# Optimization experiments

Measured on AMD Instinct MI355X. Metric: run time of the kernel, lower is better.

The kernel has to match this reference:

```python
import jax, jax.numpy as jnp
import numpy as np

B, L, D, H = 8, 1024, 1024, 16
DH = D // H  # 64


def setup_inputs() -> dict:
    key = jax.random.key(0)
    ks = jax.random.split(key, 6)
    x = jax.random.normal(ks[0], (B, L, D), dtype=jnp.float32)
    mask = jax.random.randint(ks[1], (1, L, L), 0, 2).astype(jnp.float32)
    # params initialized ~ normal(std=0.1) as in the module's _initialize
    Wk = jax.random.normal(ks[2], (D, D), dtype=jnp.float32) * 0.1
    Wv = jax.random.normal(ks[3], (D, D), dtype=jnp.float32) * 0.1
    Wq = jax.random.normal(ks[4], (D, D), dtype=jnp.float32) * 0.1
    Wo = jax.random.normal(ks[5], (D, D), dtype=jnp.float32) * 0.1
    return {"x": x, "mask": mask, "Wk": Wk, "Wv": Wv, "Wq": Wq, "Wo": Wo}


def reference(x, mask, Wk, Wv, Wq, Wo):
    # torch Linear: y = x @ W.T
    k = jnp.einsum('bld,ed->ble', x, Wk).reshape(B, L, H, DH)
    v = jnp.einsum('bld,ed->ble', x, Wv).reshape(B, L, H, DH)
    q = jnp.einsum('bld,ed->ble', x, Wq).reshape(B, L, H, DH)
    # explicit score matrix [B, H, L, L]
    scores = jnp.einsum('blhe,bmhe->bhlm', q, k)
    m = mask[:, None]  # (1, 1, L, L) broadcasts over batch and heads
    scores = scores * m - 1e9 * (1.0 - m)
    scale = np.float32(1.0 / np.sqrt(DH))
    weights = jax.nn.softmax(scores * scale, axis=-1)
    out = jnp.einsum('bhlm,bmhe->blhe', weights, v).reshape(B, L, D)
    out = jnp.einsum('bld,ed->ble', out, Wo)  # output_linear (n_heads > 1)
    return out
```

## Files before the change

kernel.cpp:

```cpp
#include <hip/hip_runtime.h>

#define B_  8
#define L_  1024
#define D_  1024
#define H_  16
#define DH_ 64

typedef unsigned short u16;
typedef __attribute__((ext_vector_type(8))) short short8;
typedef __attribute__((ext_vector_type(8))) _Float16 half8;
typedef __attribute__((ext_vector_type(4))) float floatx4;
typedef __attribute__((ext_vector_type(16))) float floatx16;

static __device__ __forceinline__ u16 f2bf(float f) {
  union { float f; unsigned u; } cv; cv.f = f;
  unsigned u = cv.u;
  return (u16)((u + 0x7fffu + ((u >> 16) & 1u)) >> 16);
}
static __device__ __forceinline__ u16 f2h(float f) {
  union { _Float16 h; u16 u; } cv; cv.h = (_Float16)f; return cv.u;
}
static __device__ __forceinline__ unsigned pack_bf2(float a, float b) {
  union { float f; unsigned u; } ua, ub; ua.f = a; ub.f = b;
  return __builtin_amdgcn_perm(ub.u + 0x8000u, ua.u + 0x8000u, 0x07060302u);
}

__global__ void cast_all(const float* __restrict__ x,  const float* __restrict__ wq,
                         const float* __restrict__ wk, const float* __restrict__ wv,
                         const float* __restrict__ wo, const float* __restrict__ mask,
                         u16* __restrict__ xf,  u16* __restrict__ wqf,
                         u16* __restrict__ wkf, u16* __restrict__ wvf,
                         u16* __restrict__ wof, float* __restrict__ biasP) {
  int blk = blockIdx.x;
  if (blk >= 12288) {
    int i = (blk - 12288) * 256 + threadIdx.x;
    int e = i & 3, lane = (i >> 2) & 63, rr = (i >> 8) & 3, t = (i >> 10) & 1;
    int c = (i >> 11) & 15, w = (i >> 15) & 3, qt = i >> 17;
    int kk  = e + 8 * rr + 4 * (lane >> 5);
    int row = qt * 128 + w * 32 + (lane & 31);
    int key = c * 64 + t * 32 + kk;
    biasP[i] = (mask[(size_t)row * L_ + key] - 1.0f) * 1.25e8f - 24.0f;
    return;
  }
  const float* src; u16* dst; int off;
  if (blk < 8192)       { src = x;  dst = xf;  off = blk; }
  else if (blk < 9216)  { src = wq; dst = wqf; off = blk - 8192; }
  else if (blk < 10240) { src = wk; dst = wkf; off = blk - 9216; }
  else if (blk < 11264) { src = wv; dst = wvf; off = blk - 10240; }
  else                  { src = wo; dst = wof; off = blk - 11264; }
  int i = off * 1024 + threadIdx.x * 4;
  float4 f = *(const float4*)(src + i);
  ushort4 r;
  r.x = f2h(f.x); r.y = f2h(f.y); r.z = f2h(f.z); r.w = f2h(f.w);
  *(ushort4*)(dst + i) = r;
}

typedef __attribute__((address_space(3))) void  lds_void;
typedef const __attribute__((address_space(1))) void g_void;
static __device__ __forceinline__ void load_lds16(const void* g, void* l) {
  __builtin_amdgcn_global_load_lds((g_void*)g, (lds_void*)l, 16, 0, 0);
}

__global__ __launch_bounds__(256) void gemm_qkv(const u16* __restrict__ A,
                                                const u16* __restrict__ wq,
                                                const u16* __restrict__ wk,
                                                const u16* __restrict__ wv,
                                                u16* __restrict__ qf,
                                                u16* __restrict__ kf,
                                                u16* __restrict__ vb) {
  const int K = D_, N = D_;
  int nb = blockIdx.x;
  const u16* Bw; u16* Cp; float scale; int obf;
  if (nb < 8)       { Bw = wq; Cp = qf; scale = 0.125f; obf = 0; }
  else if (nb < 16) { Bw = wk; Cp = kf; scale = 1.0f;   obf = 0; }
  else              { Bw = wv; Cp = vb; scale = 1.0f;   obf = 1; }
  const int n0 = (nb & 7) * 128;

  __shared__ u16 lA[128 * 32];
  __shared__ u16 lB[128 * 32];
  const int tid  = threadIdx.x;
  const int w    = tid >> 6;
  const int lane = tid & 63;
  const int m    = lane & 15;
  const int kg   = lane >> 4;
  const int m0   = blockIdx.y * 128;
  const int wm   = (w >> 1) * 64;
  const int wn   = (w & 1) * 64;
  const int rowS = tid >> 2;
  const int part = tid & 3;

  floatx4 acc[4][4];
#pragma unroll
  for (int i = 0; i < 4; ++i)
#pragma unroll
    for (int j = 0; j < 4; ++j)
#pragma unroll
      for (int r = 0; r < 4; ++r) acc[i][j][r] = 0.0f;

  for (int k0 = 0; k0 < K; k0 += 32) {
    __syncthreads();
#pragma unroll
    for (int rnd = 0; rnd < 2; ++rnd) {
      const u16* ga = A  + (size_t)(m0 + rnd * 64 + rowS) * K + k0 + part * 8;
      const u16* gb = Bw + (size_t)(n0 + rnd * 64 + rowS) * K + k0 + part * 8;
      load_lds16(ga, lA + rnd * 2048 + w * 512);
      load_lds16(gb, lB + rnd * 2048 + w * 512);
    }
    __syncthreads();

    half8 af[4], bf[4];
#pragma unroll
    for (int i = 0; i < 4; ++i) af[i] = *(const half8*)&lA[(wm + i * 16 + m) * 32 + kg * 8];
#pragma unroll
    for (int i = 0; i < 4; ++i) bf[i] = *(const half8*)&lB[(wn + i * 16 + m) * 32 + kg * 8];
#pragma unroll
    for (int mi = 0; mi < 4; ++mi)
#pragma unroll
      for (int ni = 0; ni < 4; ++ni)
        acc[mi][ni] = __builtin_amdgcn_mfma_f32_16x16x32_f16(af[mi], bf[ni], acc[mi][ni], 0, 0, 0);
  }

#pragma unroll
  for (int mi = 0; mi < 4; ++mi)
#pragma unroll
    for (int ni = 0; ni < 4; ++ni)
#pragma unroll
      for (int r = 0; r < 4; ++r) {
        int row = m0 + wm + mi * 16 + kg * 4 + r;
        int col = n0 + wn + ni * 16 + m;
        size_t idx = (size_t)row * N + col;
        float vv = acc[mi][ni][r] * scale;
        Cp[idx] = obf ? f2bf(vv) : f2h(vv);
      }
}

__global__ __launch_bounds__(256) void gemm_fin(const u16* __restrict__ A,
                                                const u16* __restrict__ Bw,
                                                float* __restrict__ Cp,
                                                int M, int N, int K) {
  __shared__ u16 lA[128 * 32];
  __shared__ u16 lB[128 * 32];
  const int tid  = threadIdx.x;
  const int w    = tid >> 6;
  const int lane = tid & 63;
  const int m    = lane & 15;
  const int kg   = lane >> 4;
  const int m0   = blockIdx.y * 128;
  const int n0   = blockIdx.x * 128;
  const int wm   = (w >> 1) * 64;
  const int wn   = (w & 1) * 64;
  const int rowS = tid >> 2;
  const int part = tid & 3;

  floatx4 acc[4][4];
#pragma unroll
  for (int i = 0; i < 4; ++i)
#pragma unroll
    for (int j = 0; j < 4; ++j)
#pragma unroll
      for (int r = 0; r < 4; ++r) acc[i][j][r] = 0.0f;

  for (int k0 = 0; k0 < K; k0 += 32) {
    __syncthreads();
#pragma unroll
    for (int rnd = 0; rnd < 2; ++rnd) {
      const u16* ga = A  + (size_t)(m0 + rnd * 64 + rowS) * K + k0 + part * 8;
      const u16* gb = Bw + (size_t)(n0 + rnd * 64 + rowS) * K + k0 + part * 8;
      load_lds16(ga, lA + rnd * 2048 + w * 512);
      load_lds16(gb, lB + rnd * 2048 + w * 512);
    }
    __syncthreads();

    half8 af[4], bf[4];
#pragma unroll
    for (int i = 0; i < 4; ++i) af[i] = *(const half8*)&lA[(wm + i * 16 + m) * 32 + kg * 8];
#pragma unroll
    for (int i = 0; i < 4; ++i) bf[i] = *(const half8*)&lB[(wn + i * 16 + m) * 32 + kg * 8];
#pragma unroll
    for (int mi = 0; mi < 4; ++mi)
#pragma unroll
      for (int ni = 0; ni < 4; ++ni)
        acc[mi][ni] = __builtin_amdgcn_mfma_f32_16x16x32_f16(af[mi], bf[ni], acc[mi][ni], 0, 0, 0);
  }

#pragma unroll
  for (int mi = 0; mi < 4; ++mi)
#pragma unroll
    for (int ni = 0; ni < 4; ++ni)
#pragma unroll
      for (int r = 0; r < 4; ++r) {
        int row = m0 + wm + mi * 16 + kg * 4 + r;
        int col = n0 + wn + ni * 16 + m;
        Cp[(size_t)row * N + col] = acc[mi][ni][r];
      }
}

__global__ __launch_bounds__(256) void transpose_v(const u16* __restrict__ v,
                                                   u16* __restrict__ vt) {
  __shared__ u16 lds[64][72];
  const int b  = blockIdx.y >> 4;
  const int h  = blockIdx.y & 15;
  const int l0 = blockIdx.x * 64;
  const int tid = threadIdx.x;
#pragma unroll
  for (int it = 0; it < 2; ++it) {
    int idx = it * 256 + tid;
    int i = idx >> 3, off = (idx & 7) * 8;
    *(short8*)&lds[i][off] =
        *(const short8*)(v + ((size_t)(b * L_ + l0 + i)) * D_ + h * 64 + off);
  }
  __syncthreads();
  const int j  = tid >> 2;
  const int p0 = (tid & 3) * 16;
  __attribute__((aligned(16))) u16 tmp[16];
#pragma unroll
  for (int s = 0; s < 16; ++s) {
    int p = p0 + s;
    int l = (p >> 1) + ((p & 1) << 5);
    tmp[s] = lds[l][j];
  }
  u16* dst = vt + ((size_t)((b * H_ + h) * DH_ + j)) * L_ + l0 + p0;
  *(short8*)(dst)     = *(const short8*)&tmp[0];
  *(short8*)(dst + 8) = *(const short8*)&tmp[8];
}

__global__ __launch_bounds__(256) void attn_kernel(const u16* __restrict__ q,
                                                   const u16* __restrict__ k,
                                                   const u16* __restrict__ vt,
                                                   const float* __restrict__ biasP,
                                                   u16* __restrict__ o) {
  __shared__ u16 lK[64][72];
  __shared__ u16 lVt[64][72];

  const int bh = blockIdx.x, qt = blockIdx.y;
  const int b = bh >> 4, h = bh & 15;
  const int tid = threadIdx.x;
  const int w = tid >> 6, lane = tid & 63;
  const int c32 = lane & 31, hi = lane >> 5;
  const int qr0 = qt * 128 + w * 32;

  const int srow  = tid >> 3;
  const int skoff = (tid & 7) * 8;

  const size_t qbase = ((size_t)((b * L_ + qr0 + c32) * H_ + h)) * DH_;
  half8 aq[4];
#pragma unroll
  for (int ks = 0; ks < 4; ++ks)
    aq[ks] = *(const half8*)(q + qbase + ks * 16 + hi * 8);

  floatx16 acc0, acc1, sumacc;
#pragma unroll
  for (int i = 0; i < 16; ++i) { acc0[i] = 0.0f; acc1[i] = 0.0f; sumacc[i] = 0.0f; }

  short8 ones;
#pragma unroll
  for (int j = 0; j < 8; ++j) ones[j] = (short)0x3F80;

  short8 rk[2], rv[2];
#pragma unroll
  for (int it = 0; it < 2; ++it) {
    rk[it] = *(const short8*)(k + ((size_t)((b * L_ + it * 32 + srow) * H_ + h)) * DH_ + skoff);
    rv[it] = *(const short8*)(vt + ((size_t)((b * H_ + h) * DH_ + it * 32 + srow)) * L_ + skoff);
  }

  const float4* bias4 = (const float4*)(biasP + ((size_t)(qt * 4 + w) * 16) * 2048) + lane;
  float4 bb[8];
#pragma unroll
  for (int r = 0; r < 8; ++r) bb[r] = bias4[r * 64];

  for (int c = 0; c < 16; ++c) {
    __syncthreads();
#pragma unroll
    for (int it = 0; it < 2; ++it) {
      *(short8*)&lK[it * 32 + srow][skoff]  = rk[it];
      *(short8*)&lVt[it * 32 + srow][skoff] = rv[it];
    }
    __syncthreads();

    if (c < 15) {
      const int nb2 = (c + 1) * 64;
#pragma unroll
      for (int it = 0; it < 2; ++it) {
        rk[it] = *(const short8*)(k + ((size_t)((b * L_ + nb2 + it * 32 + srow) * H_ + h)) * DH_ + skoff);
        rv[it] = *(const short8*)(vt + ((size_t)((b * H_ + h) * DH_ + it * 32 + srow)) * L_ + nb2 + skoff);
      }
    }

    floatx16 s0, s1;
#pragma unroll
    for (int rr = 0; rr < 4; ++rr) {
      float4 b0 = bb[rr];
      float4 b1 = bb[rr + 4];
      s0[rr * 4 + 0] = b0.x; s0[rr * 4 + 1] = b0.y; s0[rr * 4 + 2] = b0.z; s0[rr * 4 + 3] = b0.w;
      s1[rr * 4 + 0] = b1.x; s1[rr * 4 + 1] = b1.y; s1[rr * 4 + 2] = b1.z; s1[rr * 4 + 3] = b1.w;
    }
    if (c < 15) {
      const float4* bp = bias4 + (size_t)(c + 1) * 512;
#pragma unroll
      for (int r = 0; r < 8; ++r) bb[r] = bp[r * 64];
    }

#pragma unroll
    for (int ks = 0; ks < 4; ++ks) {
      half8 bk0 = *(const half8*)&lK[c32][ks * 16 + hi * 8];
      half8 bk1 = *(const half8*)&lK[32 + c32][ks * 16 + hi * 8];
      s0 = __builtin_amdgcn_mfma_f32_32x32x16_f16(bk0, aq[ks], s0, 0, 0, 0);
      s1 = __builtin_amdgcn_mfma_f32_32x32x16_f16(bk1, aq[ks], s1, 0, 0, 0);
    }

    union { short8 v[4]; unsigned u[16]; } ap;
#pragma unroll
    for (int reg = 0; reg < 16; ++reg) {
      float p0 = __expf(s0[reg]);
      float p1 = __expf(s1[reg]);
      ap.u[reg] = pack_bf2(p0, p1);
    }

#pragma unroll
    for (int ks = 0; ks < 4; ++ks) {
      short8 bv0 = *(const short8*)&lVt[c32][ks * 16 + hi * 8];
      short8 bv1 = *(const short8*)&lVt[32 + c32][ks * 16 + hi * 8];
      acc0   = __builtin_amdgcn_mfma_f32_32x32x16_bf16(ap.v[ks], bv0, acc0, 0, 0, 0);
      acc1   = __builtin_amdgcn_mfma_f32_32x32x16_bf16(ap.v[ks], bv1, acc1, 0, 0, 0);
      sumacc = __builtin_amdgcn_mfma_f32_32x32x16_bf16(ap.v[ks], ones, sumacc, 0, 0, 0);
    }
  }

#pragma unroll
  for (int reg = 0; reg < 16; ++reg) {
    int row = qr0 + (reg & 3) + 8 * (reg >> 2) + 4 * hi;
    float inv = 1.0f / sumacc[reg];
    size_t obase = ((size_t)((b * L_ + row) * H_ + h)) * DH_;
    o[obase + c32]      = f2h(acc0[reg] * inv);
    o[obase + 32 + c32] = f2h(acc1[reg] * inv);
  }
}

extern "C" void kernel_launch(void* const* d_in, const int* in_sizes, int n_in,
                              void* d_out, int out_size, void* d_ws, size_t ws_size,
                              hipStream_t stream) {
  const float* x    = (const float*)d_in[0];
  const float* mask = (const float*)d_in[1];
  const float* Wk   = (const float*)d_in[2];
  const float* Wv   = (const float*)d_in[3];
  const float* Wq   = (const float*)d_in[4];
  const float* Wo   = (const float*)d_in[5];

  char* ws = (char*)d_ws;
  u16* xf    = (u16*)(ws);
  u16* aout  = xf;
  u16* kf    = (u16*)(ws + (16ull << 20));
  u16* vtb   = (u16*)(ws + (32ull << 20));
  float* biasP = (float*)(ws + (48ull << 20));
  u16* wqf   = (u16*)(ws + (52ull << 20));
  u16* wkf   = (u16*)(ws + (54ull << 20));
  u16* wvf   = (u16*)(ws + (56ull << 20));
  u16* wof   = (u16*)(ws + (58ull << 20));
  u16* qf = (u16*)d_out;
  u16* vb = qf + (size_t)B_ * L_ * D_;

  cast_all<<<16384, 256, 0, stream>>>(x, Wq, Wk, Wv, Wo, mask,
                                      xf, wqf, wkf, wvf, wof, biasP);

  gemm_qkv<<<dim3(24, 64), 256, 0, stream>>>(xf, wqf, wkf, wvf, qf, kf, vb);

  transpose_v<<<dim3(L_ / 64, B_ * H_), 256, 0, stream>>>(vb, vtb);

  attn_kernel<<<dim3(B_ * H_, L_ / 128), 256, 0, stream>>>(qf, kf, vtb, biasP, aout);

  gemm_fin<<<dim3(D_ / 128, (B_ * L_) / 128), 256, 0, stream>>>(
      aout, wof, (float*)d_out, B_ * L_, D_, D_);
}
```

Baseline: 270.6 us.

## Replace ones-MFMA row sum with VALU sums, use exp2 with folded log2e

The softmax denominator was computed by a third MFMA against a vector of ones. It is now accumulated per lane in fp32 during the exp loop, combined across the two half-waves with a shuffle, and passed through LDS for the final normalisation, which removes a third of the PV-stage MFMAs. The exponent now uses a native exp2, with log2(e) folded into the Q scale and into the mask bias constants. The bias register prefetch is dropped in favour of direct loads each iteration, and launch bounds request 4 blocks per CU to raise occupancy. The risks are exposed bias-load latency and a row sum taken from unrounded probabilities while the numerator uses bf16-rounded ones.

```diff
diff --git a/kernel.cpp b/kernel.cpp
--- a/kernel.cpp
+++ b/kernel.cpp
@@ -24,6 +24,12 @@
   union { float f; unsigned u; } ua, ub; ua.f = a; ub.f = b;
   return __builtin_amdgcn_perm(ub.u + 0x8000u, ua.u + 0x8000u, 0x07060302u);
 }
+
+#if __has_builtin(__builtin_amdgcn_exp2f)
+#define EXP2(x) __builtin_amdgcn_exp2f(x)
+#else
+#define EXP2(x) __expf((x) * 0.6931471805599453f)
+#endif
 
 __global__ void cast_all(const float* __restrict__ x,  const float* __restrict__ wq,
                          const float* __restrict__ wk, const float* __restrict__ wv,
@@ -39,7 +45,7 @@
     int kk  = e + 8 * rr + 4 * (lane >> 5);
     int row = qt * 128 + w * 32 + (lane & 31);
     int key = c * 64 + t * 32 + kk;
-    biasP[i] = (mask[(size_t)row * L_ + key] - 1.0f) * 1.25e8f - 24.0f;
+    biasP[i] = (mask[(size_t)row * L_ + key] - 1.0f) * 1.8033688e8f - 34.624681f;
     return;
   }
   const float* src; u16* dst; int off;
@@ -71,9 +77,9 @@
   const int K = D_, N = D_;
   int nb = blockIdx.x;
   const u16* Bw; u16* Cp; float scale; int obf;
-  if (nb < 8)       { Bw = wq; Cp = qf; scale = 0.125f; obf = 0; }
-  else if (nb < 16) { Bw = wk; Cp = kf; scale = 1.0f;   obf = 0; }
-  else              { Bw = wv; Cp = vb; scale = 1.0f;   obf = 1; }
+  if (nb < 8)       { Bw = wq; Cp = qf; scale = 0.18033688f; obf = 0; }
+  else if (nb < 16) { Bw = wk; Cp = kf; scale = 1.0f;        obf = 0; }
+  else              { Bw = wv; Cp = vb; scale = 1.0f;        obf = 1; }
   const int n0 = (nb & 7) * 128;
 
   __shared__ u16 lA[128 * 32];
@@ -224,13 +230,14 @@
   *(short8*)(dst + 8) = *(const short8*)&tmp[8];
 }
 
-__global__ __launch_bounds__(256) void attn_kernel(const u16* __restrict__ q,
-                                                   const u16* __restrict__ k,
-                                                   const u16* __restrict__ vt,
-                                                   const float* __restrict__ biasP,
-                                                   u16* __restrict__ o) {
+__global__ __launch_bounds__(256, 4) void attn_kernel(const u16* __restrict__ q,
+                                                      const u16* __restrict__ k,
+                                                      const u16* __restrict__ vt,
+                                                      const float* __restrict__ biasP,
+                                                      u16* __restrict__ o) {
   __shared__ u16 lK[64][72];
   __shared__ u16 lVt[64][72];
+  __shared__ float lRS[4][32];
 
   const int bh = blockIdx.x, qt = blockIdx.y;
   const int b = bh >> 4, h = bh & 15;
@@ -248,25 +255,22 @@
   for (int ks = 0; ks < 4; ++ks)
     aq[ks] = *(const half8*)(q + qbase + ks * 16 + hi * 8);
 
-  floatx16 acc0, acc1, sumacc;
-#pragma unroll
-  for (int i = 0; i < 16; ++i) { acc0[i] = 0.0f; acc1[i] = 0.0f; sumacc[i] = 0.0f; }
-
-  short8 ones;
-#pragma unroll
-  for (int j = 0; j < 8; ++j) ones[j] = (short)0x3F80;
+  floatx16 acc0, acc1;
+#pragma unroll
+  for (int i = 0; i < 16; ++i) { acc0[i] = 0.0f; acc1[i] = 0.0f; }
+  float rsum0 = 0.0f, rsum1 = 0.0f;
+
+  const u16* kp = k  + ((size_t)((b * L_ + srow) * H_ + h)) * DH_ + skoff;
+  const u16* vp = vt + ((size_t)((b * H_ + h) * DH_ + srow)) * L_ + skoff;
 
   short8 rk[2], rv[2];
 #pragma unroll
   for (int it = 0; it < 2; ++it) {
-    rk[it] = *(const short8*)(k + ((size_t)((b * L_ + it * 32 + srow) * H_ + h)) * DH_ + skoff);
-    rv[it] = *(const short8*)(vt + ((size_t)((b * H_ + h) * DH_ + it * 32 + srow)) * L_ + skoff);
-  }
-
-  const float4* bias4 = (const float4*)(biasP + ((size_t)(qt * 4 + w) * 16) * 2048) + lane;
-  float4 bb[8];
-#pragma unroll
-  for (int r = 0; r < 8; ++r) bb[r] = bias4[r * 64];
+    rk[it] = *(const short8*)(kp + (size_t)it * 32 * H_ * DH_);
+    rv[it] = *(const short8*)(vp + (size_t)it * 32 * L_);
+  }
+
+  const float4* bp = (const float4*)(biasP + ((size_t)(qt * 4 + w) * 16) * 2048) + lane;
 
   for (int c = 0; c < 16; ++c) {
     __syncthreads();
@@ -277,27 +281,24 @@
     }
     __syncthreads();
 
-    if (c < 15) {
-      const int nb2 = (c + 1) * 64;
-#pragma unroll
-      for (int it = 0; it < 2; ++it) {
-        rk[it] = *(const short8*)(k + ((size_t)((b * L_ + nb2 + it * 32 + srow) * H_ + h)) * DH_ + skoff);
-        rv[it] = *(const short8*)(vt + ((size_t)((b * H_ + h) * DH_ + it * 32 + srow)) * L_ + nb2 + skoff);
-      }
-    }
-
     floatx16 s0, s1;
 #pragma unroll
     for (int rr = 0; rr < 4; ++rr) {
-      float4 b0 = bb[rr];
-      float4 b1 = bb[rr + 4];
+      float4 b0 = bp[rr * 64];
+      float4 b1 = bp[(4 + rr) * 64];
       s0[rr * 4 + 0] = b0.x; s0[rr * 4 + 1] = b0.y; s0[rr * 4 + 2] = b0.z; s0[rr * 4 + 3] = b0.w;
       s1[rr * 4 + 0] = b1.x; s1[rr * 4 + 1] = b1.y; s1[rr * 4 + 2] = b1.z; s1[rr * 4 + 3] = b1.w;
     }
+    bp += 512;
+
     if (c < 15) {
-      const float4* bp = bias4 + (size_t)(c + 1) * 512;
-#pragma unroll
-      for (int r = 0; r < 8; ++r) bb[r] = bp[r * 64];
+      kp += (size_t)64 * H_ * DH_;
+      vp += 64;
+#pragma unroll
+      for (int it = 0; it < 2; ++it) {
+        rk[it] = *(const short8*)(kp + (size_t)it * 32 * H_ * DH_);
+        rv[it] = *(const short8*)(vp + (size_t)it * 32 * L_);
+      }
     }
 
 #pragma unroll
@@ -311,25 +312,30 @@
     union { short8 v[4]; unsigned u[16]; } ap;
 #pragma unroll
     for (int reg = 0; reg < 16; ++reg) {
-      float p0 = __expf(s0[reg]);
-      float p1 = __expf(s1[reg]);
+      float p0 = EXP2(s0[reg]);
+      float p1 = EXP2(s1[reg]);
       ap.u[reg] = pack_bf2(p0, p1);
+      if (reg & 1) rsum1 += p0 + p1; else rsum0 += p0 + p1;
     }
 
 #pragma unroll
     for (int ks = 0; ks < 4; ++ks) {
       short8 bv0 = *(const short8*)&lVt[c32][ks * 16 + hi * 8];
       short8 bv1 = *(const short8*)&lVt[32 + c32][ks * 16 + hi * 8];
-      acc0   = __builtin_amdgcn_mfma_f32_32x32x16_bf16(ap.v[ks], bv0, acc0, 0, 0, 0);
-      acc1   = __builtin_amdgcn_mfma_f32_32x32x16_bf16(ap.v[ks], bv1, acc1, 0, 0, 0);
-      sumacc = __builtin_amdgcn_mfma_f32_32x32x16_bf16(ap.v[ks], ones, sumacc, 0, 0, 0);
-    }
-  }
+      acc0 = __builtin_amdgcn_mfma_f32_32x32x16_bf16(ap.v[ks], bv0, acc0, 0, 0, 0);
+      acc1 = __builtin_amdgcn_mfma_f32_32x32x16_bf16(ap.v[ks], bv1, acc1, 0, 0, 0);
+    }
+  }
+
+  float rsum = rsum0 + rsum1;
+  rsum += __shfl_xor(rsum, 32, 64);
+  if (hi == 0) lRS[w][c32] = rsum;
 
 #pragma unroll
   for (int reg = 0; reg < 16; ++reg) {
-    int row = qr0 + (reg & 3) + 8 * (reg >> 2) + 4 * hi;
-    float inv = 1.0f / sumacc[reg];
+    int rl = (reg & 3) + 8 * (reg >> 2) + 4 * hi;
+    float inv = 1.0f / lRS[w][rl];
+    int row = qr0 + rl;
     size_t obase = ((size_t)((b * L_ + row) * H_ + h)) * DH_;
     o[obase + c32]      = f2h(acc0[reg] * inv);
     o[obase + 32 + c32] = f2h(acc1[reg] * inv);
```

Result: faster. 254.7 us (-5.9%).
